# Kernel optimization log

Hardware: AMD Instinct MI355X
Metric: run time of the kernel (lower is better)

## Reference

```python
import jax, jax.numpy as jnp
import numpy as np

N_NODES = 10000


def setup_inputs() -> dict:
    key = jax.random.key(0)
    k1, k2, k3 = jax.random.split(key, 3)
    x = jax.random.normal(k1, (N_NODES, 768), dtype=jnp.float32)
    edge_index = jax.random.randint(k2, (2, 100000), 0, N_NODES, dtype=jnp.int32)
    # GCNConv linear weight, stored [in, out] for x @ W
    W = jax.random.normal(k3, (768, 768), dtype=jnp.float32) * (1.0 / np.sqrt(768))
    b = jnp.zeros((768,), dtype=jnp.float32)
    return {"x": x, "edge_index": edge_index, "W": W, "b": b}


def reference(x, edge_index, W, b):
    # PyG GCNConv: add self-loops, symmetric degree normalization,
    # linear transform, then scatter-add aggregation (source -> target).
    n = x.shape[0]
    loops = jnp.arange(n, dtype=edge_index.dtype)
    row = jnp.concatenate([edge_index[0], loops])  # source nodes  [E+N]
    col = jnp.concatenate([edge_index[1], loops])  # target nodes  [E+N]

    ones = jnp.ones(row.shape[0], dtype=x.dtype)
    deg = jax.ops.segment_sum(ones, col, num_segments=n)          # in-degree incl. self-loop
    dinv = jnp.where(deg > 0, jax.lax.rsqrt(deg), 0.0)
    norm = dinv[row] * dinv[col]                                   # [E+N]

    h = x @ W                                                      # [N, out]
    msg = h[row] * norm[:, None]                                   # gather + scale
    out = jax.ops.segment_sum(msg, col, num_segments=n) + b        # scatter-add
    return out
```

## Files before the change

### kernel.cpp

```cpp
#include <hip/hip_runtime.h>
#include <hip/hip_bf16.h>
#include <stdint.h>

#define DIM 768
#define BM 128
#define BN 128
#define BK 64
#define SMAX 64
#define FILL_BLOCKS 64

typedef __attribute__((ext_vector_type(8))) short short8;
typedef __attribute__((ext_vector_type(4))) float f32x4;

__device__ __forceinline__ void gload_lds16(const void* g, void* l) {
  __builtin_amdgcn_global_load_lds(
      (const __attribute__((address_space(1))) void*)g,
      (__attribute__((address_space(3))) void*)l, 16, 0, 0);
}

__device__ __forceinline__ unsigned short f2bf(float f) {
  union { __hip_bfloat16 h; unsigned short u; } cv;
  cv.h = __float2bfloat16(f);
  return cv.u;
}

__device__ __forceinline__ float bf2f(unsigned short u) {
  return __uint_as_float(((unsigned)u) << 16);
}


#define WT_TILES 576
#define CVTX_BLOCKS 3750

__global__ __launch_bounds__(256) void prep_kernel(
    const float* __restrict__ x, const float* __restrict__ W,
    unsigned short* __restrict__ xbf, unsigned short* __restrict__ wt,
    int* __restrict__ cnt, int N) {
  __shared__ float tile[32][33];
  const int b = blockIdx.x;
  const int t = threadIdx.x;
  if (b < WT_TILES) {
    int bx = b % (DIM / 32), by = b / (DIM / 32);
    int n0 = bx * 32, k0 = by * 32;
    int tx = t & 31, ty = t >> 5;
#pragma unroll
    for (int i = 0; i < 4; ++i) {
      int r = ty + i * 8;
      tile[r][tx] = W[(size_t)(k0 + r) * DIM + n0 + tx];
    }
    __syncthreads();
#pragma unroll
    for (int i = 0; i < 4; ++i) {
      int r = ty + i * 8;
      wt[(size_t)(n0 + r) * DIM + k0 + tx] = f2bf(tile[tx][r]);
    }
  } else if (b < WT_TILES + CVTX_BLOCKS) {
    int i = (b - WT_TILES) * 256 + t;
    if (i < N * DIM / 8) {
      const float4* xp = ((const float4*)x) + (size_t)i * 2;
      float4 v0 = xp[0], v1 = xp[1];
      ushort4 o0, o1;
      o0.x = f2bf(v0.x); o0.y = f2bf(v0.y); o0.z = f2bf(v0.z); o0.w = f2bf(v0.w);
      o1.x = f2bf(v1.x); o1.y = f2bf(v1.y); o1.z = f2bf(v1.z); o1.w = f2bf(v1.w);
      ushort4* op = ((ushort4*)xbf) + (size_t)i * 2;
      op[0] = o0; op[1] = o1;
    }
  } else {
    int i = (b - WT_TILES - CVTX_BLOCKS) * 256 + t;
#pragma unroll
    for (int j = 0; j < 4; ++j) {
      int idx = i * 4 + j;
      if (idx < N) cnt[idx] = 0;
    }
  }
}


__global__ __launch_bounds__(256) void gemm_fill_kernel(
    const unsigned short* __restrict__ xbf, const unsigned short* __restrict__ wt,
    unsigned short* __restrict__ g, int M,
    const int* __restrict__ row, const int* __restrict__ col, int E,
    int* __restrict__ cnt, int* __restrict__ srcs, int gemmBlocks) {
  __shared__ __align__(16) unsigned short Als[BM * BK];
  __shared__ __align__(16) unsigned short Bls[BN * BK];
  const int t = threadIdx.x;

  if ((int)blockIdx.x >= gemmBlocks) {
    int i0 = ((int)blockIdx.x - gemmBlocks) * 256 + t;
    for (int i = i0; i < E; i += FILL_BLOCKS * 256) {
      int c = col[i];
      int pos = atomicAdd(&cnt[c], 1);
      if (pos < SMAX) srcs[c * SMAX + pos] = row[i];
    }
    return;
  }

  int fid = blockIdx.x;
  int q = gemmBlocks >> 3, r8 = gemmBlocks & 7;
  int xcd = fid & 7, ii = fid >> 3;
  int nid = (xcd < r8 ? xcd * (q + 1) : r8 * (q + 1) + (xcd - r8) * q) + ii;
  const int tile_m = (nid / (DIM / BN)) * BM;
  const int n0 = (nid % (DIM / BN)) * BN;

  const int lane = t & 63;
  const int w = t >> 6;
  const int wr = w >> 1, wc = w & 1;

  f32x4 acc[4][4];
#pragma unroll
  for (int i = 0; i < 4; ++i)
#pragma unroll
    for (int j = 0; j < 4; ++j) acc[i][j] = (f32x4){0.f, 0.f, 0.f, 0.f};

  for (int kt = 0; kt < DIM / BK; ++kt) {
    const int k0 = kt * BK;
    __syncthreads();
#pragma unroll
    for (int it = 0; it < 4; ++it) {
      int p = it * 256 + t;
      int r = p >> 3;
      int gl = (p & 7) ^ (r & 7);
      int ga = tile_m + r;
      if (ga > M - 1) ga = M - 1;
      gload_lds16(xbf + (size_t)ga * DIM + k0 + gl * 8, (char*)Als + p * 16);
      gload_lds16(wt + (size_t)(n0 + r) * DIM + k0 + gl * 8, (char*)Bls + p * 16);
    }
    __syncthreads();

#pragma unroll
    for (int kk = 0; kk < 2; ++kk) {
      short8 a[4], b[4];
#pragma unroll
      for (int mi = 0; mi < 4; ++mi) {
        int r = wr * 64 + mi * 16 + (lane & 15);
        int ch = kk * 4 + (lane >> 4);
        a[mi] = *(const short8*)((const char*)Als + r * 128 + ((ch ^ (r & 7)) * 16));
      }
#pragma unroll
      for (int ni = 0; ni < 4; ++ni) {
        int c = wc * 64 + ni * 16 + (lane & 15);
        int ch = kk * 4 + (lane >> 4);
        b[ni] = *(const short8*)((const char*)Bls + c * 128 + ((ch ^ (c & 7)) * 16));
      }
#pragma unroll
      for (int mi = 0; mi < 4; ++mi)
#pragma unroll
        for (int ni = 0; ni < 4; ++ni)
          acc[mi][ni] = __builtin_amdgcn_mfma_f32_16x16x32_bf16(a[mi], b[ni], acc[mi][ni], 0, 0, 0);
    }
  }

#pragma unroll
  for (int mi = 0; mi < 4; ++mi) {
#pragma unroll
    for (int reg = 0; reg < 4; ++reg) {
      int m = tile_m + wr * 64 + mi * 16 + (lane >> 4) * 4 + reg;
      if (m < M) {
#pragma unroll
        for (int ni = 0; ni < 4; ++ni) {
          int n = n0 + wc * 64 + ni * 16 + (lane & 15);
          g[(size_t)m * DIM + n] = f2bf(acc[mi][ni][reg]);
        }
      }
    }
  }
}


__global__ __launch_bounds__(192) void agg_kernel(
    const unsigned short* __restrict__ g, const int* __restrict__ cnt,
    const int* __restrict__ srcs, const float* __restrict__ b,
    float* __restrict__ out) {
  __shared__ int sidx[SMAX];
  __shared__ float sdsc[SMAX];
  int c = blockIdx.x;
  int t = threadIdx.x;
  int deg = cnt[c];
  if (deg > SMAX) deg = SMAX;
  if (t < deg) {
    int s = srcs[c * SMAX + t];
    sidx[t] = s;
    sdsc[t] = rsqrtf((float)cnt[s] + 1.0f);
  }
  float dv = rsqrtf((float)deg + 1.0f);
  const ushort4* gr = (const ushort4*)(g + (size_t)c * DIM);
  ushort4 v = gr[t];
  float a0 = dv * bf2f(v.x), a1 = dv * bf2f(v.y);
  float a2 = dv * bf2f(v.z), a3 = dv * bf2f(v.w);
  __syncthreads();
  int j = 0;
  for (; j + 4 <= deg; j += 4) {
    int i0 = sidx[j], i1 = sidx[j + 1], i2 = sidx[j + 2], i3 = sidx[j + 3];
    float d0 = sdsc[j], d1 = sdsc[j + 1], d2 = sdsc[j + 2], d3 = sdsc[j + 3];
    ushort4 u0 = ((const ushort4*)(g + (size_t)i0 * DIM))[t];
    ushort4 u1 = ((const ushort4*)(g + (size_t)i1 * DIM))[t];
    ushort4 u2 = ((const ushort4*)(g + (size_t)i2 * DIM))[t];
    ushort4 u3 = ((const ushort4*)(g + (size_t)i3 * DIM))[t];
    a0 += d0 * bf2f(u0.x) + d1 * bf2f(u1.x) + d2 * bf2f(u2.x) + d3 * bf2f(u3.x);
    a1 += d0 * bf2f(u0.y) + d1 * bf2f(u1.y) + d2 * bf2f(u2.y) + d3 * bf2f(u3.y);
    a2 += d0 * bf2f(u0.z) + d1 * bf2f(u1.z) + d2 * bf2f(u2.z) + d3 * bf2f(u3.z);
    a3 += d0 * bf2f(u0.w) + d1 * bf2f(u1.w) + d2 * bf2f(u2.w) + d3 * bf2f(u3.w);
  }
  for (; j < deg; ++j) {
    float dj = sdsc[j];
    ushort4 u = ((const ushort4*)(g + (size_t)sidx[j] * DIM))[t];
    a0 += dj * bf2f(u.x); a1 += dj * bf2f(u.y);
    a2 += dj * bf2f(u.z); a3 += dj * bf2f(u.w);
  }
  float4 bb = ((const float4*)b)[t];
  float4 r;
  r.x = dv * a0 + bb.x;
  r.y = dv * a1 + bb.y;
  r.z = dv * a2 + bb.z;
  r.w = dv * a3 + bb.w;
  ((float4*)(out + (size_t)c * DIM))[t] = r;
}


extern "C" void kernel_launch(void* const* d_in, const int* in_sizes, int n_in,
                              void* d_out, int out_size, void* d_ws, size_t ws_size,
                              hipStream_t stream) {
  const float* x = (const float*)d_in[0];
  const int* ei = (const int*)d_in[1];
  const float* W = (const float*)d_in[2];
  const float* b = (const float*)d_in[3];
  float* out = (float*)d_out;
  const int N = in_sizes[0] / DIM;
  const int E = in_sizes[1] / 2;
  const int* row = ei;
  const int* col = ei + E;

  char* ws = (char*)d_ws;
  size_t off = 0;
  auto alloc = [&](size_t bytes) {
    size_t o = off;
    off = (off + bytes + 15) & ~(size_t)15;
    return o;
  };
  int* cnt   = (int*)(ws + alloc((size_t)N * 4));
  int* srcs  = (int*)(ws + alloc((size_t)N * SMAX * 4));
  unsigned short* xbf = (unsigned short*)(ws + alloc((size_t)N * DIM * 2));
  unsigned short* wt  = (unsigned short*)(ws + alloc((size_t)DIM * DIM * 2));
  unsigned short* g   = (unsigned short*)(ws + alloc((size_t)N * DIM * 2));

  int zero_blocks = (N + 1023) / 1024;
  int gemm_blocks = ((N + BM - 1) / BM) * (DIM / BN);

  prep_kernel<<<WT_TILES + CVTX_BLOCKS + zero_blocks, 256, 0, stream>>>(
      x, W, xbf, wt, cnt, N);
  gemm_fill_kernel<<<gemm_blocks + FILL_BLOCKS, 256, 0, stream>>>(
      xbf, wt, g, N, row, col, E, cnt, srcs, gemm_blocks);
  agg_kernel<<<N, 192, 0, stream>>>(g, cnt, srcs, b, out);
}
```

Baseline: 63.71 us.

## Fuse x fp32-to-bf16 conversion into GEMM A-tile loading

Drops the separate pass that converts x to a bf16 buffer. The GEMM now loads fp32 x tiles straight into LDS with a 16-chunk XOR swizzle and converts them to bf16 while building the MFMA operands. This removes a full write and re-read of the bf16 copy of x. In exchange it doubles LDS use for the A tile to 32KB, doubles the global A traffic per tile, since the 6 column blocks each re-read fp32 x, and adds conversion instructions to the inner loop.

```diff
diff --git a/kernel.cpp b/kernel.cpp
--- a/kernel.cpp
+++ b/kernel.cpp
@@ -30,11 +30,9 @@
 
 
 #define WT_TILES 576
-#define CVTX_BLOCKS 3750
 
 __global__ __launch_bounds__(256) void prep_kernel(
-    const float* __restrict__ x, const float* __restrict__ W,
-    unsigned short* __restrict__ xbf, unsigned short* __restrict__ wt,
+    const float* __restrict__ W, unsigned short* __restrict__ wt,
     int* __restrict__ cnt, int N) {
   __shared__ float tile[32][33];
   const int b = blockIdx.x;
@@ -54,19 +52,8 @@
       int r = ty + i * 8;
       wt[(size_t)(n0 + r) * DIM + k0 + tx] = f2bf(tile[tx][r]);
     }
-  } else if (b < WT_TILES + CVTX_BLOCKS) {
+  } else {
     int i = (b - WT_TILES) * 256 + t;
-    if (i < N * DIM / 8) {
-      const float4* xp = ((const float4*)x) + (size_t)i * 2;
-      float4 v0 = xp[0], v1 = xp[1];
-      ushort4 o0, o1;
-      o0.x = f2bf(v0.x); o0.y = f2bf(v0.y); o0.z = f2bf(v0.z); o0.w = f2bf(v0.w);
-      o1.x = f2bf(v1.x); o1.y = f2bf(v1.y); o1.z = f2bf(v1.z); o1.w = f2bf(v1.w);
-      ushort4* op = ((ushort4*)xbf) + (size_t)i * 2;
-      op[0] = o0; op[1] = o1;
-    }
-  } else {
-    int i = (b - WT_TILES - CVTX_BLOCKS) * 256 + t;
 #pragma unroll
     for (int j = 0; j < 4; ++j) {
       int idx = i * 4 + j;
@@ -77,11 +64,11 @@
 
 
 __global__ __launch_bounds__(256) void gemm_fill_kernel(
-    const unsigned short* __restrict__ xbf, const unsigned short* __restrict__ wt,
+    const float* __restrict__ x, const unsigned short* __restrict__ wt,
     unsigned short* __restrict__ g, int M,
     const int* __restrict__ row, const int* __restrict__ col, int E,
     int* __restrict__ cnt, int* __restrict__ srcs, int gemmBlocks) {
-  __shared__ __align__(16) unsigned short Als[BM * BK];
+  __shared__ __align__(16) float Alsf[BM * BK];
   __shared__ __align__(16) unsigned short Bls[BN * BK];
   const int t = threadIdx.x;
 
@@ -116,13 +103,20 @@
     const int k0 = kt * BK;
     __syncthreads();
 #pragma unroll
+    for (int it = 0; it < 8; ++it) {
+      int p = it * 256 + t;
+      int r = p >> 4;
+      int c = p & 15;
+      int gl = c ^ (r & 15);
+      int ga = tile_m + r;
+      if (ga > M - 1) ga = M - 1;
+      gload_lds16(x + (size_t)ga * DIM + k0 + gl * 4, (char*)Alsf + p * 16);
+    }
+#pragma unroll
     for (int it = 0; it < 4; ++it) {
       int p = it * 256 + t;
       int r = p >> 3;
       int gl = (p & 7) ^ (r & 7);
-      int ga = tile_m + r;
-      if (ga > M - 1) ga = M - 1;
-      gload_lds16(xbf + (size_t)ga * DIM + k0 + gl * 8, (char*)Als + p * 16);
       gload_lds16(wt + (size_t)(n0 + r) * DIM + k0 + gl * 8, (char*)Bls + p * 16);
     }
     __syncthreads();
@@ -133,8 +127,15 @@
 #pragma unroll
       for (int mi = 0; mi < 4; ++mi) {
         int r = wr * 64 + mi * 16 + (lane & 15);
-        int ch = kk * 4 + (lane >> 4);
-        a[mi] = *(const short8*)((const char*)Als + r * 128 + ((ch ^ (r & 7)) * 16));
+        int cc = (kk * 4 + (lane >> 4)) * 2;
+        f32x4 lo = *(const f32x4*)((const char*)Alsf + r * 256 + ((cc ^ (r & 15)) * 16));
+        f32x4 hi = *(const f32x4*)((const char*)Alsf + r * 256 + (((cc + 1) ^ (r & 15)) * 16));
+        short8 av;
+        av[0] = (short)f2bf(lo[0]); av[1] = (short)f2bf(lo[1]);
+        av[2] = (short)f2bf(lo[2]); av[3] = (short)f2bf(lo[3]);
+        av[4] = (short)f2bf(hi[0]); av[5] = (short)f2bf(hi[1]);
+        av[6] = (short)f2bf(hi[2]); av[7] = (short)f2bf(hi[3]);
+        a[mi] = av;
       }
 #pragma unroll
       for (int ni = 0; ni < 4; ++ni) {
@@ -239,16 +240,14 @@
   };
   int* cnt   = (int*)(ws + alloc((size_t)N * 4));
   int* srcs  = (int*)(ws + alloc((size_t)N * SMAX * 4));
-  unsigned short* xbf = (unsigned short*)(ws + alloc((size_t)N * DIM * 2));
-  unsigned short* wt  = (unsigned short*)(ws + alloc((size_t)DIM * DIM * 2));
-  unsigned short* g   = (unsigned short*)(ws + alloc((size_t)N * DIM * 2));
+  unsigned short* wt = (unsigned short*)(ws + alloc((size_t)DIM * DIM * 2));
+  unsigned short* g  = (unsigned short*)(ws + alloc((size_t)N * DIM * 2));
 
   int zero_blocks = (N + 1023) / 1024;
   int gemm_blocks = ((N + BM - 1) / BM) * (DIM / BN);
 
-  prep_kernel<<<WT_TILES + CVTX_BLOCKS + zero_blocks, 256, 0, stream>>>(
-      x, W, xbf, wt, cnt, N);
+  prep_kernel<<<WT_TILES + zero_blocks, 256, 0, stream>>>(W, wt, cnt, N);
   gemm_fill_kernel<<<gemm_blocks + FILL_BLOCKS, 256, 0, stream>>>(
-      xbf, wt, g, N, row, col, E, cnt, srcs, gemm_blocks);
+      x, wt, g, N, row, col, E, cnt, srcs, gemm_blocks);
   agg_kernel<<<N, 192, 0, stream>>>(g, cnt, srcs, b, out);
 }
```

Measured after the change: 61.64 us. -3.2%, faster.
